# Performance work log

Measured on AMD Instinct MI355X. Metric: run time of the kernel, lower is better.

## Reference

```python
import jax, jax.numpy as jnp
import numpy as np

N = 10000   # nodes
E = 100000  # edges
B = 64      # graphs
HID = 128


def setup_inputs() -> dict:
    key = jax.random.key(0)
    ks = iter(jax.random.split(key, 64))
    def nrm(shape, s=0.1):
        return jax.random.normal(next(ks), shape, dtype=jnp.float32) * s
    inp = {}
    inp["x"] = nrm((N, 1), 1.0)
    inp["node_type"] = jax.random.randint(next(ks), (N,), 0, 2)
    inp["edge_index"] = jax.random.randint(next(ks), (2, E), 0, N)
    inp["edge_attr"] = nrm((E, 1), 1.0)
    inp["batch"] = jnp.sort(jax.random.randint(next(ks), (N,), 0, B))
    inp["vp_w"] = nrm((1, HID)); inp["vp_b"] = nrm((HID,))
    inp["type_emb"] = nrm((2, HID))
    def conv(pre, fin, h, c):
        inp[pre + "_wl"] = nrm((fin, h * c)); inp[pre + "_bl"] = nrm((h * c,))
        inp[pre + "_wr"] = nrm((fin, h * c)); inp[pre + "_br"] = nrm((h * c,))
        inp[pre + "_we"] = nrm((1, h * c));  inp[pre + "_att"] = nrm((h, c))
        inp[pre + "_bias"] = nrm((h * c if pre != "c3" else c,))
    conv("c1", HID, 8, HID)
    conv("c2", HID * 8, 2, HID)
    conv("c3", HID * 2, 1, HID)
    inp["m1_w"] = nrm((HID, HID)); inp["m1_b"] = nrm((HID,))
    inp["ln1_g"] = jnp.ones((HID,), jnp.float32); inp["ln1_b"] = jnp.zeros((HID,), jnp.float32)
    inp["m2_w"] = nrm((HID, HID // 2)); inp["m2_b"] = nrm((HID // 2,))
    inp["ln2_g"] = jnp.ones((HID // 2,), jnp.float32); inp["ln2_b"] = jnp.zeros((HID // 2,), jnp.float32)
    inp["m3_w"] = nrm((HID // 2, 1)); inp["m3_b"] = nrm((1,))
    return inp


def _gatv2(x, src, dst, ea, wl, bl, wr, br, we, att, bias, heads, out_ch, concat):
    """PyG GATv2Conv (eval mode): add self-loops (edge_attr fill='mean' over dst),
    attn = (att * leaky_relu(Wl x_src + Wr x_dst + We e)).sum(-1), segment-softmax
    over destination, scatter-add of alpha * Wl x_src."""
    n = x.shape[0]
    ones = jnp.ones((ea.shape[0], 1), ea.dtype)
    deg = jax.ops.segment_sum(ones, dst, num_segments=n)
    loop_attr = jax.ops.segment_sum(ea, dst, num_segments=n) / jnp.maximum(deg, 1.0)
    ar = jnp.arange(n, dtype=src.dtype)
    src2 = jnp.concatenate([src, ar])
    dst2 = jnp.concatenate([dst, ar])
    ea2 = jnp.concatenate([ea, loop_attr], axis=0)
    xl = (x @ wl + bl).reshape(n, heads, out_ch)   # source transform
    xr = (x @ wr + br).reshape(n, heads, out_ch)   # target transform
    e = (ea2 @ we).reshape(-1, heads, out_ch)      # [E2, H, C]
    msg = xl[src2]                                 # [E2, H, C]
    z = jax.nn.leaky_relu(msg + xr[dst2] + e, 0.2)
    score = jnp.einsum('ehc,hc->eh', z, att)       # [E2, H]
    smax = jax.ops.segment_max(score, dst2, num_segments=n)
    ex = jnp.exp(score - smax[dst2])
    denom = jax.ops.segment_sum(ex, dst2, num_segments=n)
    alpha = ex / denom[dst2]
    out = jax.ops.segment_sum(alpha[:, :, None] * msg, dst2, num_segments=n)
    out = out.reshape(n, heads * out_ch) if concat else out.mean(axis=1)
    return out + bias


def _layernorm(v, g, b):
    mu = v.mean(-1, keepdims=True)
    var = v.var(-1, keepdims=True)
    return (v - mu) / jnp.sqrt(var + 1e-5) * g + b


def reference(x, node_type, edge_index, edge_attr, batch,
              vp_w, vp_b, type_emb,
              c1_wl, c1_bl, c1_wr, c1_br, c1_we, c1_att, c1_bias,
              c2_wl, c2_bl, c2_wr, c2_br, c2_we, c2_att, c2_bias,
              c3_wl, c3_bl, c3_wr, c3_br, c3_we, c3_att, c3_bias,
              m1_w, m1_b, ln1_g, ln1_b, m2_w, m2_b, ln2_g, ln2_b, m3_w, m3_b):
    src, dst = edge_index[0], edge_index[1]
    h = x @ vp_w + vp_b + type_emb[node_type]
    h = jax.nn.leaky_relu(_gatv2(h, src, dst, edge_attr, c1_wl, c1_bl, c1_wr, c1_br, c1_we, c1_att, c1_bias, 8, HID, True), 0.2)
    h = jax.nn.leaky_relu(_gatv2(h, src, dst, edge_attr, c2_wl, c2_bl, c2_wr, c2_br, c2_we, c2_att, c2_bias, 2, HID, True), 0.2)
    h = jax.nn.leaky_relu(_gatv2(h, src, dst, edge_attr, c3_wl, c3_bl, c3_wr, c3_br, c3_we, c3_att, c3_bias, 1, HID, False), 0.2)
    # masked global mean pool over node_type == 0
    w = (node_type == 0).astype(h.dtype)
    sums = jax.ops.segment_sum(h * w[:, None], batch, num_segments=B)
    cnts = jax.ops.segment_sum(w, batch, num_segments=B)
    pooled = sums / jnp.maximum(cnts, 1.0)[:, None]
    h1 = jax.nn.leaky_relu(_layernorm(pooled @ m1_w + m1_b, ln1_g, ln1_b), 0.2)
    h2 = jax.nn.leaky_relu(_layernorm(h1 @ m2_w + m2_b, ln2_g, ln2_b), 0.2)
    return (h2 @ m3_w + m3_b).squeeze(-1)
```

## Files before the change

kernel.cpp:

```cpp
#include <hip/hip_runtime.h>
#include <math.h>

#define NN 10000
#define NE 100000
#define E2 (NE + NN)
#define NBATCH 64

typedef short bf16x8 __attribute__((ext_vector_type(8)));
typedef float f32x4 __attribute__((ext_vector_type(4)));

__device__ __forceinline__ float lrelu(float v){ return fmaxf(v, 0.2f*v); }

__device__ __forceinline__ unsigned short f2bf(float x){
  unsigned int u = __float_as_uint(x);
  u += 0x7fffu + ((u >> 16) & 1u);
  return (unsigned short)(u >> 16);
}
__device__ __forceinline__ float bf2f(unsigned short u){
  return __uint_as_float(((unsigned int)u) << 16);
}

__global__ __launch_bounds__(256) void prep_kernel(
    const float* __restrict__ vp_w, const float* __restrict__ vp_b,
    const float* __restrict__ type_emb,
    const float* __restrict__ c1_wl, const float* __restrict__ c1_bl,
    const float* __restrict__ c1_wr, const float* __restrict__ c1_br,
    float* __restrict__ Ul, float* __restrict__ CTl,
    float* __restrict__ Ur, float* __restrict__ CTr,
    const float* __restrict__ c2_wl, const float* __restrict__ c2_wr,
    const float* __restrict__ c3_wl, const float* __restrict__ c3_wr,
    unsigned short* __restrict__ W2lT, unsigned short* __restrict__ W2rT,
    unsigned short* __restrict__ W3lT, unsigned short* __restrict__ W3rT,
    float* __restrict__ zbase, int zero_words)
{
  __shared__ float t[64][65];
  int b = blockIdx.x;
  int tid = threadIdx.x;
  if (b < 144){
    const float* in; unsigned short* out; int K, N, idx;
    if (b < 64)      { in=c2_wl; out=W2lT; K=1024; N=256; idx=b; }
    else if (b <128) { in=c2_wr; out=W2rT; K=1024; N=256; idx=b-64; }
    else if (b <136) { in=c3_wl; out=W3lT; K=256;  N=128; idx=b-128; }
    else             { in=c3_wr; out=W3rT; K=256;  N=128; idx=b-136; }
    int K64 = K >> 6;
    int kx = idx % K64, nx = idx / K64;
    int k0 = kx*64, n0 = nx*64;
    int lr = tid >> 4;
    int lc = (tid & 15) * 4;
#pragma unroll
    for (int i=0;i<4;++i){
      int r = lr + i*16;
      float4 v = *(const float4*)(in + (size_t)(k0+r)*N + n0 + lc);
      t[r][lc+0]=v.x; t[r][lc+1]=v.y; t[r][lc+2]=v.z; t[r][lc+3]=v.w;
    }
    __syncthreads();
    int sr = tid >> 3;
    int sc = (tid & 7) * 8;
#pragma unroll
    for (int i=0;i<2;++i){
      int n = sr + i*32;
      unsigned short tmp[8];
#pragma unroll
      for (int j=0;j<8;++j) tmp[j] = f2bf(t[sc+j][n]);
      unsigned short* op = out + (size_t)(n0+n)*K + k0 + sc;
      *(ushort4*)op       = make_ushort4(tmp[0],tmp[1],tmp[2],tmp[3]);
      *(ushort4*)(op + 4) = make_ushort4(tmp[4],tmp[5],tmp[6],tmp[7]);
    }
  } else if (b < 148){
    int j = (b-144)*256 + tid;
    float ul=0.f, c0l=0.f, c1l=0.f, ur=0.f, c0r=0.f, c1r=0.f;
    for (int k=0; k<128; ++k){
      float a = c1_wl[k*1024 + j], bb = c1_wr[k*1024 + j];
      float vw = vp_w[k], vb = vp_b[k], t0 = type_emb[k], t1 = type_emb[128+k];
      ul += vw*a; ur += vw*bb;
      c0l += (vb+t0)*a; c1l += (vb+t1)*a;
      c0r += (vb+t0)*bb; c1r += (vb+t1)*bb;
    }
    float bl = c1_bl[j], br = c1_br[j];
    Ul[j]=ul; Ur[j]=ur;
    CTl[j]      = c0l + bl;
    CTl[1024+j] = c1l + bl;
    CTr[j]      = c0r + br;
    CTr[1024+j] = c1r + br;
  } else {
    for (int i = (b-148)*256 + tid; i < zero_words; i += 32*256)
      zbase[i] = 0.f;
  }
}

__global__ void count_kernel(const int* __restrict__ dst, const float* __restrict__ ea,
                             int* __restrict__ deg, float* __restrict__ loop_sum){
  int e = blockIdx.x*256 + threadIdx.x;
  if (e < NE){
    int d = dst[e];
    atomicAdd(&deg[d], 1);
    atomicAdd(&loop_sum[d], ea[e]);
  }
}

__global__ __launch_bounds__(1024) void scan_kernel(const int* __restrict__ deg,
    const float* __restrict__ loop_sum, int* __restrict__ rowptr, float* __restrict__ loop_attr){
  __shared__ int wsum[16];
  __shared__ int carry_s;
  int tid = threadIdx.x;
  int lane = tid & 63, wid = tid >> 6;
  if (tid == 0) carry_s = 0;
  __syncthreads();
  for (int base = 0; base < NN; base += 1024){
    int i = base + tid;
    int v = (i < NN) ? deg[i] : 0;
    int incl = v;
#pragma unroll
    for (int off = 1; off < 64; off <<= 1){
      int t = __shfl_up(incl, off, 64);
      if (lane >= off) incl += t;
    }
    if (lane == 63) wsum[wid] = incl;
    __syncthreads();
    int pre = carry_s;
    for (int w = 0; w < wid; ++w) pre += wsum[w];
    if (i < NN){
      rowptr[i] = pre + incl - v;
      loop_attr[i] = loop_sum[i] / fmaxf((float)v, 1.f);
    }
    __syncthreads();
    if (tid == 0){
      int t = 0;
      for (int w = 0; w < 16; ++w) t += wsum[w];
      carry_s += t;
    }
    __syncthreads();
  }
  if (tid == 0) rowptr[NN] = carry_s;
}

__global__ void fill_kernel(const int* __restrict__ src, const int* __restrict__ dst,
                            const float* __restrict__ ea, const int* __restrict__ rowptr,
                            int* __restrict__ rowctr, int* __restrict__ srcs,
                            float* __restrict__ eav){
  int e = blockIdx.x*256 + threadIdx.x;
  if (e < NE){
    int d = dst[e];
    int p = rowptr[d] + atomicAdd(&rowctr[d], 1);
    srcs[p] = src[e];
    eav[p] = ea[e];
  }
}

__global__ __launch_bounds__(256) void conv1_fused(
    const int* __restrict__ rowptr, const int* __restrict__ srcs,
    const float* __restrict__ eav, const float* __restrict__ loop_attr,
    const float* __restrict__ x, const int* __restrict__ ntype,
    const float* __restrict__ Ul, const float* __restrict__ Ur,
    const float* __restrict__ CTl, const float* __restrict__ CTr,
    const float* __restrict__ we, const float* __restrict__ att,
    const float* __restrict__ bias, unsigned short* __restrict__ out)
{
  int n = blockIdx.x*2 + (threadIdx.x >> 7);
  if (n >= NN) return;
  int te = threadIdx.x & 127;
  int ch0 = te * 8;
  float ul[8], we8[8], atv[8], ctl0[8], ctl1[8], cn[8];
#pragma unroll
  for (int v=0; v<8; ++v){
    ul[v]=Ul[ch0+v]; we8[v]=we[ch0+v]; atv[v]=att[ch0+v];
    ctl0[v]=CTl[ch0+v]; ctl1[v]=CTl[1024+ch0+v];
  }
  int beg = rowptr[n], deg = rowptr[n+1]-beg;
  float xn = x[n]; int tn = ntype[n]; float la = loop_attr[n];
  {
    const float* ctr = tn ? (CTr+1024) : CTr;
#pragma unroll
    for (int v=0; v<8; ++v) cn[v] = fmaf(xn, Ur[ch0+v], ctr[ch0+v]);
  }
  float m = -1e30f, l = 0.f, s1 = 0.f, s20 = 0.f;
  int   sc = (deg>0) ? srcs[beg] : n;
  float ec = (deg>0) ? eav[beg]  : la;
  float xsc = x[sc]; int tsc = ntype[sc];
  for (int idx=0; idx<=deg; ++idx){
    int nx = idx+1;
    int sn2; float en2;
    if (nx < deg){ sn2 = srcs[beg+nx]; en2 = eav[beg+nx]; }
    else         { sn2 = n;            en2 = la; }
    float xsn = x[sn2]; int tsn = ntype[sn2];
    float acc = 0.f;
#pragma unroll
    for (int v=0; v<8; ++v){
      float t = cn[v] + (tsc ? ctl1[v] : ctl0[v]);
      float z = fmaf(xsc, ul[v], fmaf(ec, we8[v], t));
      acc = fmaf(atv[v], fmaxf(z, 0.2f*z), acc);
    }
#pragma unroll
    for (int mm=1; mm<16; mm<<=1) acc += __shfl_xor(acc, mm, 16);
    float w0 = (tsc == 0) ? 1.f : 0.f;
    float mn = fmaxf(m, acc), f = __expf(m-mn), pe = __expf(acc-mn);
    l = l*f + pe; s1 = s1*f + pe*xsc; s20 = s20*f + pe*w0; m = mn;
    sc = sn2; ec = en2; xsc = xsn; tsc = tsn;
  }
  float inv = 1.f/l;
  s1 *= inv; s20 *= inv;
  float s21 = 1.f - s20;
  float4 bi0 = *(const float4*)(bias + ch0);
  float4 bi1 = *(const float4*)(bias + ch0 + 4);
  float bv[8] = {bi0.x,bi0.y,bi0.z,bi0.w,bi1.x,bi1.y,bi1.z,bi1.w};
  unsigned short o[8];
#pragma unroll
  for (int v=0; v<8; ++v)
    o[v] = f2bf(lrelu(s1*ul[v] + s20*ctl0[v] + s21*ctl1[v] + bv[v]));
  *(ushort4*)(out + (size_t)n*1024 + ch0)     = make_ushort4(o[0],o[1],o[2],o[3]);
  *(ushort4*)(out + (size_t)n*1024 + ch0 + 4) = make_ushort4(o[4],o[5],o[6],o[7]);
}

template<int H, int NPB, int VPT, bool ONLY0, bool OUTBF, bool INBF>
__global__ __launch_bounds__(64*NPB) void conv_kernel(
    const int* __restrict__ rowptr, const int* __restrict__ srcs, const float* __restrict__ eav,
    const float* __restrict__ loop_attr, const int* __restrict__ ntype,
    const void* __restrict__ Xv, int stride, int xr_off,
    const float* __restrict__ we, const float* __restrict__ att, const float* __restrict__ bias,
    void* __restrict__ out)
{
  const int HC = 64*VPT;
  const int TPH = 64/H;
  int n = blockIdx.x*NPB + (threadIdx.x >> 6);
  if (n >= NN) return;
  if (ONLY0 && ntype[n] != 0) return;
  int tid = threadIdx.x & 63;
  int ch0 = tid * VPT;
  const float* Xf = (const float*)Xv;
  const unsigned short* Xb = (const unsigned short*)Xv;
  float wev[VPT], atv[VPT], biv[VPT], xrv[VPT];
#pragma unroll
  for (int v=0; v<VPT; ++v){
    int ch = ch0+v;
    wev[v]=we[ch]; atv[v]=att[ch]; biv[v]=bias[ch];
  }
  if constexpr (INBF){
    ushort4 q = *(const ushort4*)(Xb + (size_t)n*stride + xr_off + ch0);
    xrv[0]=bf2f(q.x); xrv[1]=bf2f(q.y); xrv[2]=bf2f(q.z); xrv[3]=bf2f(q.w);
  } else {
#pragma unroll
    for (int v=0; v<VPT; ++v) xrv[v]=Xf[(size_t)n*stride + xr_off + ch0+v];
  }
  float ms[4], ls[4], A[4][VPT];
#pragma unroll
  for (int k=0; k<4; ++k){
    ms[k] = -INFINITY; ls[k] = 0.f;
#pragma unroll
    for (int v=0; v<VPT; ++v) A[k][v] = 0.f;
  }
  int beg=rowptr[n], end=rowptr[n+1];
  float la = loop_attr[n];
  for (int j=beg; j<=end; j+=4){
    bool val[4]; int sx[4]; float ex[4];
#pragma unroll
    for (int k=0; k<4; ++k){
      int pos = j + k;
      val[k] = pos <= end;
      sx[k] = (!val[k] || pos == end) ? n : srcs[pos];
      ex[k] = !val[k] ? 0.f : (pos == end ? la : eav[pos]);
    }
    float xv[4][VPT];
#pragma unroll
    for (int k=0; k<4; ++k){
      if constexpr (INBF){
        ushort4 q = *(const ushort4*)(Xb + (size_t)sx[k]*stride + ch0);
        xv[k][0]=bf2f(q.x); xv[k][1]=bf2f(q.y); xv[k][2]=bf2f(q.z); xv[k][3]=bf2f(q.w);
      } else if constexpr (VPT == 4){
        float4 q = *(const float4*)(Xf + (size_t)sx[k]*stride + ch0);
        xv[k][0]=q.x; xv[k][1]=q.y; xv[k][2]=q.z; xv[k][3]=q.w;
      } else {
        float2 q = *(const float2*)(Xf + (size_t)sx[k]*stride + ch0);
        xv[k][0]=q.x; xv[k][1]=q.y;
      }
    }
    float p[4];
#pragma unroll
    for (int k=0; k<4; ++k){
      float acc = 0.f;
#pragma unroll
      for (int v=0; v<VPT; ++v)
        acc += atv[v]*lrelu(xv[k][v]+xrv[v]+ex[k]*wev[v]);
      p[k] = acc;
    }
#pragma unroll
    for (int mm=1; mm<TPH; mm<<=1){
#pragma unroll
      for (int k=0; k<4; ++k) p[k] += __shfl_xor(p[k], mm, 64);
    }
#pragma unroll
    for (int k=0; k<4; ++k){
      if (val[k]){
        float mn=fmaxf(ms[k],p[k]), sc=__expf(ms[k]-mn), pe=__expf(p[k]-mn);
        ls[k]=ls[k]*sc+pe; ms[k]=mn;
#pragma unroll
        for (int v=0; v<VPT; ++v) A[k][v]=A[k][v]*sc+pe*xv[k][v];
      }
    }
  }
#pragma unroll
  for (int k=1; k<4; ++k){
    float mn = fmaxf(ms[0], ms[k]);
    float fa = __expf(ms[0]-mn), fb = __expf(ms[k]-mn);
    ls[0] = ls[0]*fa + ls[k]*fb;
#pragma unroll
    for (int v=0; v<VPT; ++v) A[0][v] = A[0][v]*fa + A[k][v]*fb;
    ms[0] = mn;
  }
  float inv = 1.f/ls[0];
  size_t baseo=(size_t)n*HC+ch0;
  if constexpr (OUTBF){
    unsigned short* ob = (unsigned short*)out;
    ushort4 o;
    o.x = f2bf(lrelu(A[0][0]*inv+biv[0]));
    o.y = f2bf(lrelu(A[0][1]*inv+biv[1]));
    o.z = f2bf(lrelu(A[0][2]*inv+biv[2]));
    o.w = f2bf(lrelu(A[0][3]*inv+biv[3]));
    *(ushort4*)(ob + baseo) = o;
  } else {
    float* of = (float*)out;
#pragma unroll
    for (int v=0; v<VPT; ++v) of[baseo+v]=lrelu(A[0][v]*inv+biv[v]);
  }
}

template<bool OUTBF>
__global__ __launch_bounds__(256) void gemm_dual_lds(
    const short* __restrict__ Abf,
    const short* __restrict__ WlT, const short* __restrict__ WrT,
    const float* __restrict__ bl, const float* __restrict__ br,
    void* __restrict__ Out, int M, int K, int NcH, int cgrid, int rgrid)
{
  __shared__ short lds[12288];
  int id = blockIdx.x;
  int xcd = id & 7, slot = id >> 3;
  int nb = slot % cgrid;
  int rowgroup = (slot / cgrid) * 8 + xcd;
  if (rowgroup >= rgrid) return;
  int row0 = rowgroup * 128;
  int NC2 = 2*NcH;
  int halfx = NcH >> 6;
  int isR = nb >= halfx;
  const short* WT = isR ? WrT : WlT;
  const float* bias = isR ? br : bl;
  int col0 = (nb - (isR ? halfx : 0)) * 64;
  int gcol0 = nb * 64;
  int tid = threadIdx.x;
  int lane = tid & 63, wave = tid >> 6;
  int wm = wave >> 1, wn = wave & 1;
  int quad = lane >> 4, l16 = lane & 15;

  const short* asrc[4];
#pragma unroll
  for (int i=0;i<4;++i){
    int c = wave*256 + i*64 + lane;
    int m = c >> 3, j = c & 7;
    int gr = row0 + m; gr = gr < M ? gr : M-1;
    asrc[i] = Abf + (size_t)gr*K + ((j ^ (m & 7)) << 3);
  }
  const short* bsrc[2];
#pragma unroll
  for (int i=0;i<2;++i){
    int c = wave*128 + i*64 + lane;
    int nloc = c >> 3, j = c & 7;
    bsrc[i] = WT + (size_t)(col0 + nloc)*K + ((j ^ (nloc & 7)) << 3);
  }

  float biasv[2] = { bias[col0 + wn*32 + l16], bias[col0 + wn*32 + 16 + l16] };
  f32x4 acc[4][2];
#pragma unroll
  for (int f=0; f<4; ++f)
#pragma unroll
    for (int g=0; g<2; ++g) acc[f][g] = (f32x4){0.f,0.f,0.f,0.f};

  int niter = K >> 6;
  for (int it=0; it<niter; ++it){
    int k0 = it << 6;
#pragma unroll
    for (int i=0;i<4;++i)
      __builtin_amdgcn_global_load_lds(asrc[i] + k0, &lds[(wave*256 + i*64)*8], 16, 0, 0);
#pragma unroll
    for (int i=0;i<2;++i)
      __builtin_amdgcn_global_load_lds(bsrc[i] + k0, &lds[8192 + (wave*128 + i*64)*8], 16, 0, 0);
    __syncthreads();
#pragma unroll
    for (int s=0; s<2; ++s){
      int t = s*4 + quad;
      bf16x8 af[4], bfv[2];
#pragma unroll
      for (int f=0; f<4; ++f){
        int m = wm*64 + f*16 + l16;
        af[f] = *(const bf16x8*)&lds[m*64 + ((t ^ (m & 7)) << 3)];
      }
#pragma unroll
      for (int g=0; g<2; ++g){
        int nloc = wn*32 + g*16 + l16;
        bfv[g] = *(const bf16x8*)&lds[8192 + nloc*64 + ((t ^ (nloc & 7)) << 3)];
      }
#pragma unroll
      for (int f=0; f<4; ++f)
#pragma unroll
        for (int g=0; g<2; ++g)
          acc[f][g] = __builtin_amdgcn_mfma_f32_16x16x32_bf16(af[f], bfv[g], acc[f][g], 0,0,0);
    }
    __syncthreads();
  }

#pragma unroll
  for (int f=0; f<4; ++f){
    int rbase = row0 + wm*64 + f*16 + quad*4;
#pragma unroll
    for (int r=0; r<4; ++r){
      int rr = rbase + r;
      if (rr < M){
#pragma unroll
        for (int g=0; g<2; ++g){
          int cc = gcol0 + wn*32 + g*16 + l16;
          float val = acc[f][g][r] + biasv[g];
          if constexpr (OUTBF) ((unsigned short*)Out)[(size_t)rr*NC2 + cc] = f2bf(val);
          else                 ((float*)Out)[(size_t)rr*NC2 + cc] = val;
        }
      }
    }
  }
}

__device__ __forceinline__ int lbound(const int* __restrict__ a, int n, int key){
  int lo = 0, hi = n;
  while (lo < hi){ int mid = (lo+hi) >> 1; if (a[mid] < key) lo = mid+1; else hi = mid; }
  return lo;
}

__global__ __launch_bounds__(128) void head_kernel(
    const float* __restrict__ h3, const int* __restrict__ ntype, const int* __restrict__ batch,
    const float* __restrict__ m1w, const float* __restrict__ m1b,
    const float* __restrict__ g1, const float* __restrict__ b1,
    const float* __restrict__ m2w, const float* __restrict__ m2b,
    const float* __restrict__ g2, const float* __restrict__ b2,
    const float* __restrict__ m3w, const float* __restrict__ m3b,
    float* __restrict__ out)
{
  __shared__ float p[128];
  __shared__ float hb[128];
  __shared__ float red[128];
  int b = blockIdx.x, j = threadIdx.x;
  int lo = lbound(batch, NN, b);
  int hi = lbound(batch, NN, b+1);
  float s = 0.f, cnt = 0.f;
  int n = lo;
  for (; n + 3 < hi; n += 4){
    float w0 = (ntype[n]   == 0) ? 1.f : 0.f;
    float w1 = (ntype[n+1] == 0) ? 1.f : 0.f;
    float w2 = (ntype[n+2] == 0) ? 1.f : 0.f;
    float w3 = (ntype[n+3] == 0) ? 1.f : 0.f;
    s += w0*h3[(size_t)n*128 + j]     + w1*h3[(size_t)(n+1)*128 + j]
       + w2*h3[(size_t)(n+2)*128 + j] + w3*h3[(size_t)(n+3)*128 + j];
    cnt += w0 + w1 + w2 + w3;
  }
  for (; n < hi; ++n){
    float w = (ntype[n] == 0) ? 1.f : 0.f;
    s += w*h3[(size_t)n*128 + j];
    cnt += w;
  }
  p[j] = s / fmaxf(cnt, 1.f);
  __syncthreads();
  float a = m1b[j];
  for (int k=0; k<128; ++k) a += p[k]*m1w[k*128 + j];
  red[j] = a; __syncthreads();
  for (int off=64; off>0; off>>=1){ if (j<off) red[j] += red[j+off]; __syncthreads(); }
  float mu = red[0] * (1.f/128.f);
  __syncthreads();
  float d = a - mu;
  red[j] = d*d; __syncthreads();
  for (int off=64; off>0; off>>=1){ if (j<off) red[j] += red[j+off]; __syncthreads(); }
  float var = red[0] * (1.f/128.f);
  __syncthreads();
  hb[j] = lrelu(d * rsqrtf(var + 1e-5f) * g1[j] + b1[j]);
  __syncthreads();
  float a2 = 0.f;
  if (j < 64){
    a2 = m2b[j];
    for (int k=0; k<128; ++k) a2 += hb[k]*m2w[k*64 + j];
  }
  red[j] = (j<64) ? a2 : 0.f; __syncthreads();
  for (int off=64; off>0; off>>=1){ if (j<off) red[j] += red[j+off]; __syncthreads(); }
  float mu2 = red[0] * (1.f/64.f);
  __syncthreads();
  float d2 = a2 - mu2;
  red[j] = (j<64) ? d2*d2 : 0.f; __syncthreads();
  for (int off=64; off>0; off>>=1){ if (j<off) red[j] += red[j+off]; __syncthreads(); }
  float var2 = red[0] * (1.f/64.f);
  __syncthreads();
  if (j < 64) hb[j] = lrelu(d2 * rsqrtf(var2 + 1e-5f) * g2[j] + b2[j]);
  __syncthreads();
  if (j == 0){
    float o = m3b[0];
    for (int k=0; k<64; ++k) o += hb[k]*m3w[k];
    out[b] = o;
  }
}

extern "C" void kernel_launch(void* const* d_in, const int* in_sizes, int n_in,
                              void* d_out, int out_size, void* d_ws, size_t ws_size,
                              hipStream_t stream)
{
  const float* x        = (const float*)d_in[0];
  const int*   ntype    = (const int*)d_in[1];
  const int*   ei       = (const int*)d_in[2];
  const float* eattr    = (const float*)d_in[3];
  const int*   batch    = (const int*)d_in[4];
  const float* vp_w     = (const float*)d_in[5];
  const float* vp_b     = (const float*)d_in[6];
  const float* type_emb = (const float*)d_in[7];
  const float* c1_wl = (const float*)d_in[8];  const float* c1_bl = (const float*)d_in[9];
  const float* c1_wr = (const float*)d_in[10]; const float* c1_br = (const float*)d_in[11];
  const float* c1_we = (const float*)d_in[12]; const float* c1_att= (const float*)d_in[13];
  const float* c1_bias=(const float*)d_in[14];
  const float* c2_wl = (const float*)d_in[15]; const float* c2_bl = (const float*)d_in[16];
  const float* c2_wr = (const float*)d_in[17]; const float* c2_br = (const float*)d_in[18];
  const float* c2_we = (const float*)d_in[19]; const float* c2_att= (const float*)d_in[20];
  const float* c2_bias=(const float*)d_in[21];
  const float* c3_wl = (const float*)d_in[22]; const float* c3_bl = (const float*)d_in[23];
  const float* c3_wr = (const float*)d_in[24]; const float* c3_br = (const float*)d_in[25];
  const float* c3_we = (const float*)d_in[26]; const float* c3_att= (const float*)d_in[27];
  const float* c3_bias=(const float*)d_in[28];
  const float* m1_w = (const float*)d_in[29]; const float* m1_b = (const float*)d_in[30];
  const float* ln1_g= (const float*)d_in[31]; const float* ln1_b= (const float*)d_in[32];
  const float* m2_w = (const float*)d_in[33]; const float* m2_b = (const float*)d_in[34];
  const float* ln2_g= (const float*)d_in[35]; const float* ln2_b= (const float*)d_in[36];
  const float* m3_w = (const float*)d_in[37]; const float* m3_b = (const float*)d_in[38];
  const int* esrc = ei;
  const int* edst = ei + NE;
  float* outp = (float*)d_out;
  (void)in_sizes; (void)n_in; (void)out_size; (void)ws_size;

  char* w = (char*)d_ws;
  auto alloc = [&](size_t bytes) -> void* {
    void* p = (void*)w;
    w += (bytes + 255) & ~(size_t)255;
    return p;
  };
  unsigned short* h1bf = (unsigned short*)alloc((size_t)NN*1024*2);
  unsigned short* X2   = (unsigned short*)alloc((size_t)NN*512*2);
  unsigned short* h2bf = (unsigned short*)alloc((size_t)NN*256*2);
  float* X3   = (float*)alloc((size_t)NN*256*4);
  float* h3   = (float*)alloc((size_t)NN*128*4);
  unsigned short* W2lT = (unsigned short*)alloc((size_t)256*1024*2);
  unsigned short* W2rT = (unsigned short*)alloc((size_t)256*1024*2);
  unsigned short* W3lT = (unsigned short*)alloc((size_t)128*256*2);
  unsigned short* W3rT = (unsigned short*)alloc((size_t)128*256*2);
  float* Ul   = (float*)alloc(1024*4);
  float* CTl  = (float*)alloc(2048*4);
  float* Ur   = (float*)alloc(1024*4);
  float* CTr  = (float*)alloc(2048*4);
  const int zero_words = 3*NN;
  float* zbase = (float*)alloc((size_t)zero_words*4);
  int*   deg      = (int*)zbase;
  int*   rowctr   = (int*)(zbase + NN);
  float* loop_sum = zbase + 2*NN;
  float* loop_attr= (float*)alloc((size_t)NN*4);
  int*   rowptr   = (int*)alloc((size_t)(NN+1)*4);
  int*   srcs     = (int*)alloc((size_t)NE*4);
  float* eav      = (float*)alloc((size_t)NE*4);

  prep_kernel<<<180, 256, 0, stream>>>(vp_w, vp_b, type_emb,
      c1_wl, c1_bl, c1_wr, c1_br, Ul, CTl, Ur, CTr,
      c2_wl, c2_wr, c3_wl, c3_wr, W2lT, W2rT, W3lT, W3rT,
      zbase, zero_words);
  count_kernel<<<(NE+255)/256, 256, 0, stream>>>(edst, eattr, deg, loop_sum);
  scan_kernel<<<1, 1024, 0, stream>>>(deg, loop_sum, rowptr, loop_attr);
  fill_kernel<<<(NE+255)/256, 256, 0, stream>>>(esrc, edst, eattr, rowptr, rowctr,
                                                srcs, eav);
  conv1_fused<<<NN/2, 256, 0, stream>>>(rowptr, srcs, eav, loop_attr, x, ntype,
      Ul, Ur, CTl, CTr, c1_we, c1_att, c1_bias, h1bf);
  gemm_dual_lds<true><<<640, 256, 0, stream>>>(
      (const short*)h1bf, (const short*)W2lT, (const short*)W2rT, c2_bl, c2_br,
      (void*)X2, NN, 1024, 256, 8, 79);
  conv_kernel<2,4,4,false,true,true><<<NN/4, 256, 0, stream>>>(rowptr, srcs, eav, loop_attr, ntype,
      (const void*)X2, 512, 256, c2_we, c2_att, c2_bias, h2bf);
  gemm_dual_lds<false><<<320, 256, 0, stream>>>(
      (const short*)h2bf, (const short*)W3lT, (const short*)W3rT, c3_bl, c3_br,
      (void*)X3, NN, 256, 128, 4, 79);
  conv_kernel<1,4,2,true,false,false><<<NN/4, 256, 0, stream>>>(rowptr, srcs, eav, loop_attr, ntype,
      (const void*)X3, 256, 128, c3_we, c3_att, c3_bias, h3);
  head_kernel<<<NBATCH, 128, 0, stream>>>(h3, ntype, batch, m1_w, m1_b, ln1_g, ln1_b,
                                          m2_w, m2_b, ln2_g, ln2_b, m3_w, m3_b, outp);
}
```

Before: 316.1 us.

## Pack edge src/attr and node x/type, drop softmax max tracking, remap conv1 lanes

```diff
diff --git a/kernel.cpp b/kernel.cpp
--- a/kernel.cpp
+++ b/kernel.cpp
@@ -3,7 +3,6 @@
 
 #define NN 10000
 #define NE 100000
-#define E2 (NE + NN)
 #define NBATCH 64
 
 typedef short bf16x8 __attribute__((ext_vector_type(8)));
@@ -99,121 +98,132 @@
 }
 
 __global__ __launch_bounds__(1024) void scan_kernel(const int* __restrict__ deg,
-    const float* __restrict__ loop_sum, int* __restrict__ rowptr, float* __restrict__ loop_attr){
-  __shared__ int wsum[16];
-  __shared__ int carry_s;
+    const float* __restrict__ loop_sum, const float* __restrict__ x,
+    const int* __restrict__ ntype,
+    int* __restrict__ rowptr, float* __restrict__ loop_attr, float2* __restrict__ xt){
+  __shared__ int wtot[16];
   int tid = threadIdx.x;
   int lane = tid & 63, wid = tid >> 6;
-  if (tid == 0) carry_s = 0;
-  __syncthreads();
-  for (int base = 0; base < NN; base += 1024){
-    int i = base + tid;
+  int base = tid*10;
+  int d[10]; int run = 0;
+#pragma unroll
+  for (int j=0;j<10;++j){
+    int i = base + j;
     int v = (i < NN) ? deg[i] : 0;
-    int incl = v;
-#pragma unroll
-    for (int off = 1; off < 64; off <<= 1){
-      int t = __shfl_up(incl, off, 64);
-      if (lane >= off) incl += t;
-    }
-    if (lane == 63) wsum[wid] = incl;
-    __syncthreads();
-    int pre = carry_s;
-    for (int w = 0; w < wid; ++w) pre += wsum[w];
+    run += v; d[j] = run;
+  }
+  int T = run;
+  int incl = T;
+#pragma unroll
+  for (int off=1; off<64; off<<=1){
+    int s = __shfl_up(incl, off, 64);
+    if (lane >= off) incl += s;
+  }
+  if (lane == 63) wtot[wid] = incl;
+  __syncthreads();
+  int wpre = 0;
+  for (int w2=0; w2<wid; ++w2) wpre += wtot[w2];
+  int ebase = wpre + incl - T;
+#pragma unroll
+  for (int j=0;j<10;++j){
+    int i = base + j;
     if (i < NN){
-      rowptr[i] = pre + incl - v;
+      int v = d[j] - ((j==0) ? 0 : d[j-1]);
+      rowptr[i] = ebase + d[j] - v;
       loop_attr[i] = loop_sum[i] / fmaxf((float)v, 1.f);
-    }
-    __syncthreads();
-    if (tid == 0){
-      int t = 0;
-      for (int w = 0; w < 16; ++w) t += wsum[w];
-      carry_s += t;
-    }
-    __syncthreads();
-  }
-  if (tid == 0) rowptr[NN] = carry_s;
+      xt[i] = make_float2(x[i], (float)ntype[i]);
+    }
+  }
+  if (tid == 1023) rowptr[NN] = wpre + incl;
 }
 
 __global__ void fill_kernel(const int* __restrict__ src, const int* __restrict__ dst,
                             const float* __restrict__ ea, const int* __restrict__ rowptr,
-                            int* __restrict__ rowctr, int* __restrict__ srcs,
-                            float* __restrict__ eav){
+                            int* __restrict__ rowctr, int2* __restrict__ se){
   int e = blockIdx.x*256 + threadIdx.x;
   if (e < NE){
     int d = dst[e];
     int p = rowptr[d] + atomicAdd(&rowctr[d], 1);
-    srcs[p] = src[e];
-    eav[p] = ea[e];
+    se[p] = make_int2(src[e], __float_as_int(ea[e]));
   }
 }
 
 __global__ __launch_bounds__(256) void conv1_fused(
-    const int* __restrict__ rowptr, const int* __restrict__ srcs,
-    const float* __restrict__ eav, const float* __restrict__ loop_attr,
-    const float* __restrict__ x, const int* __restrict__ ntype,
+    const int* __restrict__ rowptr, const int2* __restrict__ se,
+    const float* __restrict__ loop_attr, const float2* __restrict__ xt,
     const float* __restrict__ Ul, const float* __restrict__ Ur,
     const float* __restrict__ CTl, const float* __restrict__ CTr,
     const float* __restrict__ we, const float* __restrict__ att,
     const float* __restrict__ bias, unsigned short* __restrict__ out)
 {
-  int n = blockIdx.x*2 + (threadIdx.x >> 7);
+  int n = blockIdx.x*4 + (threadIdx.x >> 6);
   if (n >= NN) return;
-  int te = threadIdx.x & 127;
-  int ch0 = te * 8;
-  float ul[8], we8[8], atv[8], ctl0[8], ctl1[8], cn[8];
-#pragma unroll
-  for (int v=0; v<8; ++v){
-    ul[v]=Ul[ch0+v]; we8[v]=we[ch0+v]; atv[v]=att[ch0+v];
-    ctl0[v]=CTl[ch0+v]; ctl1[v]=CTl[1024+ch0+v];
-  }
+  int lane = threadIdx.x & 63;
+  int h = lane >> 3, sub = lane & 7;
+  int ch0 = h*128 + sub*16;
+  float ul[16], wev[16], atv[16], cn0[16], cnd[16];
+#pragma unroll
+  for (int v=0; v<16; ++v){ ul[v]=Ul[ch0+v]; wev[v]=we[ch0+v]; atv[v]=att[ch0+v]; }
   int beg = rowptr[n], deg = rowptr[n+1]-beg;
-  float xn = x[n]; int tn = ntype[n]; float la = loop_attr[n];
-  {
-    const float* ctr = tn ? (CTr+1024) : CTr;
-#pragma unroll
-    for (int v=0; v<8; ++v) cn[v] = fmaf(xn, Ur[ch0+v], ctr[ch0+v]);
-  }
-  float m = -1e30f, l = 0.f, s1 = 0.f, s20 = 0.f;
-  int   sc = (deg>0) ? srcs[beg] : n;
-  float ec = (deg>0) ? eav[beg]  : la;
-  float xsc = x[sc]; int tsc = ntype[sc];
+  float2 xtn = xt[n];
+  float xn = xtn.x, tfn = xtn.y;
+  float la = loop_attr[n];
+  const float* ctr = (tfn != 0.f) ? (CTr+1024) : CTr;
+#pragma unroll
+  for (int v=0; v<16; ++v){
+    float c0 = CTl[ch0+v], c1 = CTl[1024+ch0+v];
+    cn0[v] = fmaf(xn, Ur[ch0+v], ctr[ch0+v]) + c0;
+    cnd[v] = c1 - c0;
+  }
+  const int2* sp = se + beg;
+  float l = 0.f, s1 = 0.f, st1 = 0.f;
+  int s; float ea;
+  if (deg > 0){ int2 q = sp[0]; s = q.x; ea = __int_as_float(q.y); }
+  else        { s = n; ea = la; }
+  float2 xc = xt[s];
   for (int idx=0; idx<=deg; ++idx){
     int nx = idx+1;
-    int sn2; float en2;
-    if (nx < deg){ sn2 = srcs[beg+nx]; en2 = eav[beg+nx]; }
-    else         { sn2 = n;            en2 = la; }
-    float xsn = x[sn2]; int tsn = ntype[sn2];
+    int2 qn;
+    if (nx < deg) qn = sp[nx];
+    else          qn = make_int2(n, __float_as_int(la));
+    float2 xnx = xt[qn.x];
+    float xs = xc.x, tf = xc.y;
     float acc = 0.f;
 #pragma unroll
-    for (int v=0; v<8; ++v){
-      float t = cn[v] + (tsc ? ctl1[v] : ctl0[v]);
-      float z = fmaf(xsc, ul[v], fmaf(ec, we8[v], t));
+    for (int v=0; v<16; ++v){
+      float t = fmaf(tf, cnd[v], cn0[v]);
+      float z = fmaf(xs, ul[v], fmaf(ea, wev[v], t));
       acc = fmaf(atv[v], fmaxf(z, 0.2f*z), acc);
     }
-#pragma unroll
-    for (int mm=1; mm<16; mm<<=1) acc += __shfl_xor(acc, mm, 16);
-    float w0 = (tsc == 0) ? 1.f : 0.f;
-    float mn = fmaxf(m, acc), f = __expf(m-mn), pe = __expf(acc-mn);
-    l = l*f + pe; s1 = s1*f + pe*xsc; s20 = s20*f + pe*w0; m = mn;
-    sc = sn2; ec = en2; xsc = xsn; tsc = tsn;
+    acc += __shfl_xor(acc, 1, 8);
+    acc += __shfl_xor(acc, 2, 8);
+    acc += __shfl_xor(acc, 4, 8);
+    float pe = __expf(acc);
+    l += pe;
+    s1  = fmaf(pe, xs, s1);
+    st1 = fmaf(pe, tf, st1);
+    ea = __int_as_float(qn.y); xc = xnx;
   }
   float inv = 1.f/l;
-  s1 *= inv; s20 *= inv;
-  float s21 = 1.f - s20;
-  float4 bi0 = *(const float4*)(bias + ch0);
-  float4 bi1 = *(const float4*)(bias + ch0 + 4);
-  float bv[8] = {bi0.x,bi0.y,bi0.z,bi0.w,bi1.x,bi1.y,bi1.z,bi1.w};
-  unsigned short o[8];
-#pragma unroll
-  for (int v=0; v<8; ++v)
-    o[v] = f2bf(lrelu(s1*ul[v] + s20*ctl0[v] + s21*ctl1[v] + bv[v]));
-  *(ushort4*)(out + (size_t)n*1024 + ch0)     = make_ushort4(o[0],o[1],o[2],o[3]);
-  *(ushort4*)(out + (size_t)n*1024 + ch0 + 4) = make_ushort4(o[4],o[5],o[6],o[7]);
+  s1 *= inv;
+  float s21 = st1 * inv;
+  float s20 = 1.f - s21;
+  bf16x8 w0v, w1v;
+#pragma unroll
+  for (int v=0; v<16; ++v){
+    float c0 = CTl[ch0+v], c1 = CTl[1024+ch0+v];
+    float o = lrelu(fmaf(s1, ul[v], fmaf(s20, c0, fmaf(s21, c1, bias[ch0+v]))));
+    if (v < 8) w0v[v]   = (short)f2bf(o);
+    else       w1v[v-8] = (short)f2bf(o);
+  }
+  unsigned short* op = out + (size_t)n*1024 + ch0;
+  *(bf16x8*)op       = w0v;
+  *(bf16x8*)(op + 8) = w1v;
 }
 
 template<int H, int NPB, int VPT, bool ONLY0, bool OUTBF, bool INBF>
 __global__ __launch_bounds__(64*NPB) void conv_kernel(
-    const int* __restrict__ rowptr, const int* __restrict__ srcs, const float* __restrict__ eav,
+    const int* __restrict__ rowptr, const int2* __restrict__ se,
     const float* __restrict__ loop_attr, const int* __restrict__ ntype,
     const void* __restrict__ Xv, int stride, int xr_off,
     const float* __restrict__ we, const float* __restrict__ att, const float* __restrict__ bias,
@@ -241,10 +251,10 @@
 #pragma unroll
     for (int v=0; v<VPT; ++v) xrv[v]=Xf[(size_t)n*stride + xr_off + ch0+v];
   }
-  float ms[4], ls[4], A[4][VPT];
+  float ls[4], A[4][VPT];
 #pragma unroll
   for (int k=0; k<4; ++k){
-    ms[k] = -INFINITY; ls[k] = 0.f;
+    ls[k] = 0.f;
 #pragma unroll
     for (int v=0; v<VPT; ++v) A[k][v] = 0.f;
   }
@@ -256,8 +266,10 @@
     for (int k=0; k<4; ++k){
       int pos = j + k;
       val[k] = pos <= end;
-      sx[k] = (!val[k] || pos == end) ? n : srcs[pos];
-      ex[k] = !val[k] ? 0.f : (pos == end ? la : eav[pos]);
+      int2 q;
+      if (pos < end) q = se[pos];
+      else           q = make_int2(n, __float_as_int(la));
+      sx[k] = q.x; ex[k] = __int_as_float(q.y);
     }
     float xv[4][VPT];
 #pragma unroll
@@ -289,37 +301,28 @@
     }
 #pragma unroll
     for (int k=0; k<4; ++k){
-      if (val[k]){
-        float mn=fmaxf(ms[k],p[k]), sc=__expf(ms[k]-mn), pe=__expf(p[k]-mn);
-        ls[k]=ls[k]*sc+pe; ms[k]=mn;
-#pragma unroll
-        for (int v=0; v<VPT; ++v) A[k][v]=A[k][v]*sc+pe*xv[k][v];
-      }
-    }
-  }
-#pragma unroll
-  for (int k=1; k<4; ++k){
-    float mn = fmaxf(ms[0], ms[k]);
-    float fa = __expf(ms[0]-mn), fb = __expf(ms[k]-mn);
-    ls[0] = ls[0]*fa + ls[k]*fb;
-#pragma unroll
-    for (int v=0; v<VPT; ++v) A[0][v] = A[0][v]*fa + A[k][v]*fb;
-    ms[0] = mn;
-  }
-  float inv = 1.f/ls[0];
+      float pe = val[k] ? __expf(p[k]) : 0.f;
+      ls[k] += pe;
+#pragma unroll
+      for (int v=0; v<VPT; ++v) A[k][v] = fmaf(pe, xv[k][v], A[k][v]);
+    }
+  }
+  float lt = (ls[0]+ls[1]) + (ls[2]+ls[3]);
+  float inv = 1.f/lt;
   size_t baseo=(size_t)n*HC+ch0;
   if constexpr (OUTBF){
     unsigned short* ob = (unsigned short*)out;
     ushort4 o;
-    o.x = f2bf(lrelu(A[0][0]*inv+biv[0]));
-    o.y = f2bf(lrelu(A[0][1]*inv+biv[1]));
-    o.z = f2bf(lrelu(A[0][2]*inv+biv[2]));
-    o.w = f2bf(lrelu(A[0][3]*inv+biv[3]));
+    o.x = f2bf(lrelu(((A[0][0]+A[1][0])+(A[2][0]+A[3][0]))*inv+biv[0]));
+    o.y = f2bf(lrelu(((A[0][1]+A[1][1])+(A[2][1]+A[3][1]))*inv+biv[1]));
+    o.z = f2bf(lrelu(((A[0][2]+A[1][2])+(A[2][2]+A[3][2]))*inv+biv[2]));
+    o.w = f2bf(lrelu(((A[0][3]+A[1][3])+(A[2][3]+A[3][3]))*inv+biv[3]));
     *(ushort4*)(ob + baseo) = o;
   } else {
     float* of = (float*)out;
 #pragma unroll
-    for (int v=0; v<VPT; ++v) of[baseo+v]=lrelu(A[0][v]*inv+biv[v]);
+    for (int v=0; v<VPT; ++v)
+      of[baseo+v] = lrelu(((A[0][v]+A[1][v])+(A[2][v]+A[3][v]))*inv+biv[v]);
   }
 }
 
@@ -558,29 +561,28 @@
   int*   rowctr   = (int*)(zbase + NN);
   float* loop_sum = zbase + 2*NN;
   float* loop_attr= (float*)alloc((size_t)NN*4);
+  float2* xt      = (float2*)alloc((size_t)NN*8);
   int*   rowptr   = (int*)alloc((size_t)(NN+1)*4);
-  int*   srcs     = (int*)alloc((size_t)NE*4);
-  float* eav      = (float*)alloc((size_t)NE*4);
+  int2*  se       = (int2*)alloc((size_t)NE*8);
 
   prep_kernel<<<180, 256, 0, stream>>>(vp_w, vp_b, type_emb,
       c1_wl, c1_bl, c1_wr, c1_br, Ul, CTl, Ur, CTr,
       c2_wl, c2_wr, c3_wl, c3_wr, W2lT, W2rT, W3lT, W3rT,
       zbase, zero_words);
   count_kernel<<<(NE+255)/256, 256, 0, stream>>>(edst, eattr, deg, loop_sum);
-  scan_kernel<<<1, 1024, 0, stream>>>(deg, loop_sum, rowptr, loop_attr);
-  fill_kernel<<<(NE+255)/256, 256, 0, stream>>>(esrc, edst, eattr, rowptr, rowctr,
-                                                srcs, eav);
-  conv1_fused<<<NN/2, 256, 0, stream>>>(rowptr, srcs, eav, loop_attr, x, ntype,
+  scan_kernel<<<1, 1024, 0, stream>>>(deg, loop_sum, x, ntype, rowptr, loop_attr, xt);
+  fill_kernel<<<(NE+255)/256, 256, 0, stream>>>(esrc, edst, eattr, rowptr, rowctr, se);
+  conv1_fused<<<NN/4, 256, 0, stream>>>(rowptr, se, loop_attr, xt,
       Ul, Ur, CTl, CTr, c1_we, c1_att, c1_bias, h1bf);
   gemm_dual_lds<true><<<640, 256, 0, stream>>>(
       (const short*)h1bf, (const short*)W2lT, (const short*)W2rT, c2_bl, c2_br,
       (void*)X2, NN, 1024, 256, 8, 79);
-  conv_kernel<2,4,4,false,true,true><<<NN/4, 256, 0, stream>>>(rowptr, srcs, eav, loop_attr, ntype,
+  conv_kernel<2,4,4,false,true,true><<<NN/4, 256, 0, stream>>>(rowptr, se, loop_attr, ntype,
       (const void*)X2, 512, 256, c2_we, c2_att, c2_bias, h2bf);
   gemm_dual_lds<false><<<320, 256, 0, stream>>>(
       (const short*)h2bf, (const short*)W3lT, (const short*)W3rT, c3_bl, c3_br,
       (void*)X3, NN, 256, 128, 4, 79);
-  conv_kernel<1,4,2,true,false,false><<<NN/4, 256, 0, stream>>>(rowptr, srcs, eav, loop_attr, ntype,
+  conv_kernel<1,4,2,true,false,false><<<NN/4, 256, 0, stream>>>(rowptr, se, loop_attr, ntype,
       (const void*)X3, 256, 128, c3_we, c3_att, c3_bias, h3);
   head_kernel<<<NBATCH, 128, 0, stream>>>(h3, ntype, batch, m1_w, m1_b, ln1_g, ln1_b,
                                           m2_w, m2_b, ln2_g, ln2_b, m3_w, m3_b, outp);
```

New measurement: 322.0 us. No clear change (+1.8%).
